# Kernel tuning notes

Hardware: AMD Instinct MI355X
Metric: run time of the kernel (lower is better)

## Reference

```python
import jax, jax.numpy as jnp
import numpy as np

EPS = 1e-08
N_READS = 4
CELL_WIDTH = 64


def setup_inputs() -> dict:
    key = jax.random.key(0)
    ks = jax.random.split(key, 6)
    B, N, W, R = 8, 2048, CELL_WIDTH, N_READS
    memory = jax.random.normal(ks[0], (B, N, W), dtype=jnp.float32)
    controls = jax.random.normal(ks[1], (B, R * W + R + R * 3), dtype=jnp.float32)
    ww = jax.random.uniform(ks[2], (B, N), dtype=jnp.float32)
    write_weights = ww / ww.sum(-1, keepdims=True)  # simplex, as a DNC write head yields
    prev_links = jax.random.uniform(ks[3], (B, N, N), dtype=jnp.float32)
    prev_precedence = jax.random.uniform(ks[4], (B, N), dtype=jnp.float32)
    rw = jax.random.uniform(ks[5], (B, R, N), dtype=jnp.float32)
    prev_read_weights = rw / rw.sum(-1, keepdims=True)
    return {
        "memory": memory,
        "controls": controls,
        "write_weights": write_weights,
        "prev_links": prev_links,
        "prev_precedence": prev_precedence,
        "prev_read_weights": prev_read_weights,
    }


def reference(memory, controls, write_weights, prev_links, prev_precedence, prev_read_weights):
    B, N, W = memory.shape
    R = N_READS
    # --- split controls per self.shapes: [[R, W], R, [R, 3]] ---
    keys = controls[:, : R * W].reshape(B, R, W)
    betas = 1.0 + jax.nn.softplus(controls[:, R * W : R * W + R])  # [B, R]
    gates = jax.nn.softmax(controls[:, R * W + R :].reshape(B, R, 3), axis=-1)
    # --- content addressing: cosine similarity + softmax ---
    key_norm = jnp.linalg.norm(keys, axis=-1)    # [B, R]
    mem_norm = jnp.linalg.norm(memory, axis=-1)  # [B, N]
    dots = jnp.einsum("bnw,brw->brn", memory, keys)
    scores = dots / (key_norm[:, :, None] * mem_norm[:, None, :] + EPS)
    content_weights = jax.nn.softmax(scores * betas[:, :, None], axis=-1)  # [B, R, N]
    # --- temporal link matrix update ---
    wt_i = write_weights[:, :, None]          # [B, N, 1]
    wt_j = write_weights[:, None, :]          # [B, 1, N]
    pt_j = prev_precedence[:, None, :]        # [B, 1, N]
    diag_mask = 1.0 - jnp.eye(N, dtype=memory.dtype)
    links = ((1.0 - wt_i - wt_j) * prev_links + wt_i * pt_j) * diag_mask  # [B, N, N]
    # --- forward / backward weightings from prev read weights ---
    forward_weights = jnp.einsum("bij,brj->bri", links, prev_read_weights)
    backward_weights = jnp.einsum("bij,bri->brj", links, prev_read_weights)
    # --- mix via read modes ---
    read_weights = (
        gates[..., 0:1] * forward_weights
        + gates[..., 1:2] * backward_weights
        + gates[..., 2:3] * content_weights
    )  # [B, R, N]
    # --- read vector ---
    read_vector = jnp.einsum("bnw,brn->brw", memory, read_weights)  # [B, R, W]
    return read_vector
```

## Files before the change

### kernel.cpp

```cpp
#include <hip/hip_runtime.h>
#include <math.h>

#define BB 8
#define NN 2048
#define WWID 64
#define RNUM 4
#define CTRL 272
#define EPSF 1e-8f
#define TI 32
#define TILES 64
#define CQ 4

__device__ __forceinline__ float wred_sum(float v){
#pragma unroll
  for (int m=1;m<64;m<<=1) v += __shfl_xor(v,m);
  return v;
}

__global__ __launch_bounds__(256) void k1_prep(
    const float* __restrict__ mem, const float* __restrict__ ctr,
    const float* __restrict__ ww, const float* __restrict__ prw,
    const float* __restrict__ L,
    float* __restrict__ scores, float* __restrict__ a_arr,
    float* __restrict__ Ldiag){
  int wid = threadIdx.x >> 6, lane = threadIdx.x & 63;
  int g = blockIdx.x * 4 + wid;
  int b = g >> 11, n = g & (NN-1);
  float m = mem[((size_t)(b*NN + n))*WWID + lane];
  const float* cb = ctr + b*CTRL;
  float k0 = cb[0*WWID+lane], k1 = cb[1*WWID+lane];
  float k2 = cb[2*WWID+lane], k3 = cb[3*WWID+lane];
  float s0 = m*m;
  float d0 = m*k0, d1 = m*k1, d2 = m*k2, d3 = m*k3;
  float q0 = k0*k0, q1 = k1*k1, q2 = k2*k2, q3 = k3*k3;
#pragma unroll
  for (int t=1;t<64;t<<=1){
    s0 += __shfl_xor(s0,t);
    d0 += __shfl_xor(d0,t); d1 += __shfl_xor(d1,t);
    d2 += __shfl_xor(d2,t); d3 += __shfl_xor(d3,t);
    q0 += __shfl_xor(q0,t); q1 += __shfl_xor(q1,t);
    q2 += __shfl_xor(q2,t); q3 += __shfl_xor(q3,t);
  }
  if (lane==0){
    float mn = sqrtf(s0);
    float be[4];
#pragma unroll
    for (int r=0;r<4;r++){
      float x = cb[RNUM*WWID + r];
      be[r] = 1.f + (x > 20.f ? x : log1pf(expf(x)));
    }
    scores[(b*RNUM+0)*NN+n] = d0*be[0]/(sqrtf(q0)*mn + EPSF);
    scores[(b*RNUM+1)*NN+n] = d1*be[1]/(sqrtf(q1)*mn + EPSF);
    scores[(b*RNUM+2)*NN+n] = d2*be[2]/(sqrtf(q2)*mn + EPSF);
    scores[(b*RNUM+3)*NN+n] = d3*be[3]/(sqrtf(q3)*mn + EPSF);
    Ldiag[b*NN+n] = L[((size_t)(b*NN+n))*NN + n];
  }
  if (lane < RNUM){
    int r = lane;
    a_arr[(b*RNUM+r)*NN+n] = (1.f - ww[b*NN+n]) * prw[(b*RNUM+r)*NN+n];
  }
}

__global__ __launch_bounds__(1024) void k2_head(
    const float* __restrict__ ctr, const float* __restrict__ scores,
    const float* __restrict__ ww, const float* __restrict__ prec,
    const float* __restrict__ prw, float* __restrict__ scal){
  __shared__ float redS[16], redT[16], redE[16];
  int tid=threadIdx.x, wid=tid>>6, lane=tid&63;
  int b = blockIdx.x>>2, r = blockIdx.x&3;
  const float* sc = scores + (size_t)(b*RNUM+r)*NN;
  const float* pr = prw    + (size_t)(b*RNUM+r)*NN;
  float s0=sc[tid], s1=sc[tid+1024];
  float p0=pr[tid], p1=pr[tid+1024];
  float lE = expf(s0)+expf(s1);
  float lS = prec[b*NN+tid]*p0 + prec[b*NN+tid+1024]*p1;
  float lT = ww[b*NN+tid]*p0   + ww[b*NN+tid+1024]*p1;
  lE=wred_sum(lE); lS=wred_sum(lS); lT=wred_sum(lT);
  if (lane==0){ redE[wid]=lE; redS[wid]=lS; redT[wid]=lT; }
  __syncthreads();
  if (tid==0){
    float S=0.f,T=0.f,E=0.f;
#pragma unroll
    for(int i=0;i<16;i++){ S+=redS[i]; T+=redT[i]; E+=redE[i]; }
    const float* cb = ctr + b*CTRL;
    float c0 = cb[RNUM*WWID + RNUM + r*3 + 0];
    float c1 = cb[RNUM*WWID + RNUM + r*3 + 1];
    float c2 = cb[RNUM*WWID + RNUM + r*3 + 2];
    float mg = fmaxf(c0, fmaxf(c1, c2));
    float e0 = expf(c0-mg), e1 = expf(c1-mg), e2 = expf(c2-mg);
    float inv3 = 1.f/(e0+e1+e2);
    float* s = &scal[(b*RNUM+r)*8];
    s[0]=e0*inv3; s[1]=e1*inv3; s[2]=e2*inv3;
    s[3]=S; s[4]=T; s[5]=1.f/E;
  }
}

__global__ __launch_bounds__(256) void k3_links(
    const float* __restrict__ L, const float* __restrict__ ww,
    const float* __restrict__ prw, const float* __restrict__ a_arr,
    float* __restrict__ fwd_part, float* __restrict__ part){
  __shared__ float lrow[TI][16];
  __shared__ float lcol[4096];
  int tid = threadIdx.x, wid = tid>>6, lane = tid&63;
  int bid = blockIdx.x;
  int b   = bid >> 8;
  int rem = bid & 255;
  int tile = rem >> 2, cq = rem & 3;
  int i0 = tile*TI, jbase = cq*512;
  if (tid < TI){
    int i = i0 + tid;
    lrow[tid][0] = ww[b*NN + i];
#pragma unroll
    for (int r=0;r<RNUM;r++){
      lrow[tid][4+r] = a_arr[(b*RNUM+r)*NN + i];
      lrow[tid][8+r] = prw[(b*RNUM+r)*NN + i];
    }
  }
  __syncthreads();
  float accf[32];
#pragma unroll
  for (int k=0;k<32;k++) accf[k]=0.f;

  for (int c=0;c<2;c++){
    int j0 = jbase + c*256 + lane*4;
    float4 a4[4], p4[4];
#pragma unroll
    for (int r=0;r<4;r++){
      a4[r] = *reinterpret_cast<const float4*>(&a_arr[(b*RNUM+r)*NN + j0]);
      p4[r] = *reinterpret_cast<const float4*>(&prw[(b*RNUM+r)*NN + j0]);
    }
    float4 wwj = *reinterpret_cast<const float4*>(&ww[b*NN + j0]);
    float4 cacc[4];
#pragma unroll
    for (int r=0;r<4;r++){ cacc[r].x=0.f; cacc[r].y=0.f; cacc[r].z=0.f; cacc[r].w=0.f; }

#pragma unroll
    for (int rr=0; rr<8; rr++){
      int lr = wid*8 + rr;
      int i  = i0 + lr;
      float wwi = lrow[lr][0];
      float4 ai4 = *reinterpret_cast<const float4*>(&lrow[lr][4]);
      float4 pi4 = *reinterpret_cast<const float4*>(&lrow[lr][8]);
      float4 L4 = *reinterpret_cast<const float4*>(&L[((size_t)(b*NN + i))*NN + j0]);
#pragma unroll
      for (int r=0;r<4;r++){
        float4 ar = a4[r], pr = p4[r];
        float mx_ = fmaf(-wwi, pr.x, ar.x);
        float my_ = fmaf(-wwi, pr.y, ar.y);
        float mz_ = fmaf(-wwi, pr.z, ar.z);
        float mw_ = fmaf(-wwi, pr.w, ar.w);
        float s = accf[rr*4+r];
        s = fmaf(L4.x, mx_, s); s = fmaf(L4.y, my_, s);
        s = fmaf(L4.z, mz_, s); s = fmaf(L4.w, mw_, s);
        accf[rr*4+r] = s;
        float ai = (r==0)?ai4.x:((r==1)?ai4.y:((r==2)?ai4.z:ai4.w));
        float pi = (r==0)?pi4.x:((r==1)?pi4.y:((r==2)?pi4.z:pi4.w));
        float nx_ = fmaf(-wwj.x, pi, ai);
        float ny_ = fmaf(-wwj.y, pi, ai);
        float nz_ = fmaf(-wwj.z, pi, ai);
        float nw_ = fmaf(-wwj.w, pi, ai);
        cacc[r].x = fmaf(L4.x, nx_, cacc[r].x);
        cacc[r].y = fmaf(L4.y, ny_, cacc[r].y);
        cacc[r].z = fmaf(L4.z, nz_, cacc[r].z);
        cacc[r].w = fmaf(L4.w, nw_, cacc[r].w);
      }
    }
    __syncthreads();
#pragma unroll
    for (int r=0;r<4;r++)
      *reinterpret_cast<float4*>(&lcol[wid*1024 + r*256 + lane*4]) = cacc[r];
    __syncthreads();
    float4 v; v.x=0.f; v.y=0.f; v.z=0.f; v.w=0.f;
#pragma unroll
    for (int w=0;w<4;w++){
      float4 t = *reinterpret_cast<const float4*>(&lcol[w*1024 + wid*256 + lane*4]);
      v.x+=t.x; v.y+=t.y; v.z+=t.z; v.w+=t.w;
    }
    *reinterpret_cast<float4*>(
      &part[((size_t)((b*TILES+tile)*RNUM + wid))*NN + jbase + c*256 + lane*4]) = v;
  }

#pragma unroll
  for (int k=0;k<32;k++) accf[k] += __shfl_xor(accf[k], 32);
#pragma unroll
  for (int h=16; h>=1; h>>=1){
#pragma unroll
    for (int i=0;i<h;i++){
      float a = accf[i], bb = accf[i+h];
      bool up = (lane & h) != 0;
      float lo = up ? bb : a;
      float hi = up ? a : bb;
      accf[i] = lo + __shfl_xor(hi, h);
    }
  }
  if (lane < 32){
    int k = lane;
    fwd_part[((size_t)(b*CQ + cq)*RNUM + (k&3))*NN + i0 + wid*8 + (k>>2)] = accf[0];
  }
}

__global__ __launch_bounds__(256) void k45_combine_read(
    const float* __restrict__ part, const float* __restrict__ fwd_part,
    const float* __restrict__ scores, const float* __restrict__ scal,
    const float* __restrict__ ww, const float* __restrict__ prec,
    const float* __restrict__ prw, const float* __restrict__ Ldiag,
    const float* __restrict__ mem, float* __restrict__ out){
  __shared__ float rwl[256];
  int tid = threadIdx.x;
  int b = blockIdx.x >> 5, rem = blockIdx.x & 31;
  int r = rem >> 3, nb = rem & 7;
  int n = nb*256 + tid;
  const float* s = &scal[(b*RNUM+r)*8];
  float g0=s[0], g1=s[1], g2=s[2], S=s[3], T=s[4], inv=s[5];
  const float* pp = part + ((size_t)(b*TILES)*RNUM + r)*NN + n;
  float b0=0.f,b1=0.f,b2=0.f,b3=0.f;
  for (int t=0;t<TILES;t+=4){
    b0 += pp[(size_t)(t+0)*RNUM*NN];
    b1 += pp[(size_t)(t+1)*RNUM*NN];
    b2 += pp[(size_t)(t+2)*RNUM*NN];
    b3 += pp[(size_t)(t+3)*RNUM*NN];
  }
  float bsum = (b0+b1)+(b2+b3);
  float fsum = 0.f;
#pragma unroll
  for (int cq=0;cq<CQ;cq++)
    fsum += fwd_part[((size_t)(b*CQ + cq)*RNUM + r)*NN + n];
  float wwn = ww[b*NN+n], pn = prec[b*NN+n], prn = prw[(b*RNUM+r)*NN+n];
  float Lnn = Ldiag[b*NN+n];
  float diag = (fmaf(-2.f*wwn, Lnn, Lnn) + wwn*pn) * prn;
  float fwd = fsum + wwn*S - diag;
  float bwd = bsum + pn*T - diag;
  float content = expf(scores[(b*RNUM+r)*NN+n]) * inv;
  rwl[tid] = g0*fwd + g1*bwd + g2*content;
  __syncthreads();
  int w = tid>>6, lane = tid&63;
  float acc = 0.f;
  const float* mp = mem + ((size_t)(b*NN + nb*256 + w*64))*WWID + lane;
#pragma unroll 4
  for (int q=0; q<64; q++)
    acc = fmaf(mp[(size_t)q*WWID], rwl[w*64+q], acc);
  atomicAdd(&out[(b*RNUM+r)*WWID + lane], acc);
}

extern "C" void kernel_launch(void* const* d_in, const int* in_sizes, int n_in,
                              void* d_out, int out_size, void* d_ws, size_t ws_size,
                              hipStream_t stream){
  const float* mem  = (const float*)d_in[0];
  const float* ctr  = (const float*)d_in[1];
  const float* ww   = (const float*)d_in[2];
  const float* L    = (const float*)d_in[3];
  const float* prec = (const float*)d_in[4];
  const float* prw  = (const float*)d_in[5];
  float* out = (float*)d_out;
  float* w = (float*)d_ws;

  float* scores   = w;
  float* a_arr    = scores + BB*RNUM*NN;
  float* Ldiag    = a_arr + BB*RNUM*NN;
  float* scal     = Ldiag + BB*NN;
  float* fwd_part = scal + 256;
  float* part     = fwd_part + BB*CQ*RNUM*NN;

  hipMemsetAsync(out, 0, (size_t)BB*RNUM*WWID*sizeof(float), stream);
  k1_prep<<<BB*NN/4, 256, 0, stream>>>(mem, ctr, ww, prw, L, scores, a_arr, Ldiag);
  k2_head<<<BB*RNUM, 1024, 0, stream>>>(ctr, scores, ww, prec, prw, scal);
  k3_links<<<BB*TILES*CQ, 256, 0, stream>>>(L, ww, prw, a_arr, fwd_part, part);
  k45_combine_read<<<BB*RNUM*8, 256, 0, stream>>>(part, fwd_part, scores, scal,
                                                  ww, prec, prw, Ldiag, mem, out);
}
```

Measured before the change: 250.0 us.

## Fuse head reductions into links kernel, zero output in prep, store partials as bf16

The separate head-reduction kernel is folded into the links kernel as 32 extra blocks, and the output memset moves into the first block of the prep kernel, which removes two launches. The per-tile backward partials (64 tiles × 4 reads × 2048 × 8 batches) are now written and read as bf16 rather than fp32, halving that intermediate traffic. The risk is lost precision when 64 bf16 partial sums are accumulated. The links kernel's main work reads the full 134 MB link matrix, so the launch and partial-traffic savings are small next to it.

```diff
diff --git a/kernel.cpp b/kernel.cpp
--- a/kernel.cpp
+++ b/kernel.cpp
@@ -1,4 +1,5 @@
 #include <hip/hip_runtime.h>
+#include <hip/hip_bf16.h>
 #include <math.h>
 
 #define BB 8
@@ -10,11 +11,19 @@
 #define TI 32
 #define TILES 64
 #define CQ 4
+#define K3BLKS (BB*TILES*CQ)
 
 __device__ __forceinline__ float wred_sum(float v){
 #pragma unroll
   for (int m=1;m<64;m<<=1) v += __shfl_xor(v,m);
   return v;
+}
+__device__ __forceinline__ unsigned short f2bf(float f){
+  __hip_bfloat16 h = __float2bfloat16(f);
+  return *reinterpret_cast<unsigned short*>(&h);
+}
+__device__ __forceinline__ float bf2f(unsigned short u){
+  return __uint_as_float(((unsigned)u) << 16);
 }
 
 __global__ __launch_bounds__(256) void k1_prep(
@@ -22,8 +31,14 @@
     const float* __restrict__ ww, const float* __restrict__ prw,
     const float* __restrict__ L,
     float* __restrict__ scores, float* __restrict__ a_arr,
-    float* __restrict__ Ldiag){
-  int wid = threadIdx.x >> 6, lane = threadIdx.x & 63;
+    float* __restrict__ Ldiag, float* __restrict__ out){
+  int tid = threadIdx.x;
+  if (blockIdx.x == 0){
+    float4 z = {0.f,0.f,0.f,0.f};
+    reinterpret_cast<float4*>(out)[tid]       = z;
+    reinterpret_cast<float4*>(out)[tid + 256] = z;
+  }
+  int wid = tid >> 6, lane = tid & 63;
   int g = blockIdx.x * 4 + wid;
   int b = g >> 11, n = g & (NN-1);
   float m = mem[((size_t)(b*NN + n))*WWID + lane];
@@ -61,48 +76,54 @@
   }
 }
 
-__global__ __launch_bounds__(1024) void k2_head(
-    const float* __restrict__ ctr, const float* __restrict__ scores,
-    const float* __restrict__ ww, const float* __restrict__ prec,
-    const float* __restrict__ prw, float* __restrict__ scal){
-  __shared__ float redS[16], redT[16], redE[16];
-  int tid=threadIdx.x, wid=tid>>6, lane=tid&63;
-  int b = blockIdx.x>>2, r = blockIdx.x&3;
-  const float* sc = scores + (size_t)(b*RNUM+r)*NN;
-  const float* pr = prw    + (size_t)(b*RNUM+r)*NN;
-  float s0=sc[tid], s1=sc[tid+1024];
-  float p0=pr[tid], p1=pr[tid+1024];
-  float lE = expf(s0)+expf(s1);
-  float lS = prec[b*NN+tid]*p0 + prec[b*NN+tid+1024]*p1;
-  float lT = ww[b*NN+tid]*p0   + ww[b*NN+tid+1024]*p1;
-  lE=wred_sum(lE); lS=wred_sum(lS); lT=wred_sum(lT);
-  if (lane==0){ redE[wid]=lE; redS[wid]=lS; redT[wid]=lT; }
-  __syncthreads();
-  if (tid==0){
-    float S=0.f,T=0.f,E=0.f;
-#pragma unroll
-    for(int i=0;i<16;i++){ S+=redS[i]; T+=redT[i]; E+=redE[i]; }
-    const float* cb = ctr + b*CTRL;
-    float c0 = cb[RNUM*WWID + RNUM + r*3 + 0];
-    float c1 = cb[RNUM*WWID + RNUM + r*3 + 1];
-    float c2 = cb[RNUM*WWID + RNUM + r*3 + 2];
-    float mg = fmaxf(c0, fmaxf(c1, c2));
-    float e0 = expf(c0-mg), e1 = expf(c1-mg), e2 = expf(c2-mg);
-    float inv3 = 1.f/(e0+e1+e2);
-    float* s = &scal[(b*RNUM+r)*8];
-    s[0]=e0*inv3; s[1]=e1*inv3; s[2]=e2*inv3;
-    s[3]=S; s[4]=T; s[5]=1.f/E;
-  }
-}
-
-__global__ __launch_bounds__(256) void k3_links(
+__global__ __launch_bounds__(256) void k23_links_head(
     const float* __restrict__ L, const float* __restrict__ ww,
     const float* __restrict__ prw, const float* __restrict__ a_arr,
-    float* __restrict__ fwd_part, float* __restrict__ part){
+    const float* __restrict__ ctr, const float* __restrict__ scores,
+    const float* __restrict__ prec,
+    float* __restrict__ fwd_part, unsigned short* __restrict__ part,
+    float* __restrict__ scal){
   __shared__ float lrow[TI][16];
   __shared__ float lcol[4096];
+  __shared__ float red[3][4];
   int tid = threadIdx.x, wid = tid>>6, lane = tid&63;
   int bid = blockIdx.x;
+
+  if (bid >= K3BLKS){
+    int idx = bid - K3BLKS;
+    int b = idx >> 2, r = idx & 3;
+    const float* sc = scores + (size_t)(b*RNUM+r)*NN;
+    const float* pr = prw    + (size_t)(b*RNUM+r)*NN;
+    float lE=0.f, lS=0.f, lT=0.f;
+#pragma unroll
+    for (int k=0;k<8;k++){
+      int n = tid + k*256;
+      float p = pr[n];
+      lE += expf(sc[n]);
+      lS = fmaf(prec[b*NN+n], p, lS);
+      lT = fmaf(ww[b*NN+n],   p, lT);
+    }
+    lE=wred_sum(lE); lS=wred_sum(lS); lT=wred_sum(lT);
+    if (lane==0){ red[0][wid]=lE; red[1][wid]=lS; red[2][wid]=lT; }
+    __syncthreads();
+    if (tid==0){
+      float E = red[0][0]+red[0][1]+red[0][2]+red[0][3];
+      float S = red[1][0]+red[1][1]+red[1][2]+red[1][3];
+      float T = red[2][0]+red[2][1]+red[2][2]+red[2][3];
+      const float* cb = ctr + b*CTRL;
+      float c0 = cb[RNUM*WWID + RNUM + r*3 + 0];
+      float c1 = cb[RNUM*WWID + RNUM + r*3 + 1];
+      float c2 = cb[RNUM*WWID + RNUM + r*3 + 2];
+      float mg = fmaxf(c0, fmaxf(c1, c2));
+      float e0 = expf(c0-mg), e1 = expf(c1-mg), e2 = expf(c2-mg);
+      float inv3 = 1.f/(e0+e1+e2);
+      float* s = &scal[(b*RNUM+r)*8];
+      s[0]=e0*inv3; s[1]=e1*inv3; s[2]=e2*inv3;
+      s[3]=S; s[4]=T; s[5]=1.f/E;
+    }
+    return;
+  }
+
   int b   = bid >> 8;
   int rem = bid & 255;
   int tile = rem >> 2, cq = rem & 3;
@@ -176,8 +197,10 @@
       float4 t = *reinterpret_cast<const float4*>(&lcol[w*1024 + wid*256 + lane*4]);
       v.x+=t.x; v.y+=t.y; v.z+=t.z; v.w+=t.w;
     }
-    *reinterpret_cast<float4*>(
-      &part[((size_t)((b*TILES+tile)*RNUM + wid))*NN + jbase + c*256 + lane*4]) = v;
+    ushort4 sv;
+    sv.x = f2bf(v.x); sv.y = f2bf(v.y); sv.z = f2bf(v.z); sv.w = f2bf(v.w);
+    *reinterpret_cast<ushort4*>(
+      &part[((size_t)((b*TILES+tile)*RNUM + wid))*NN + jbase + c*256 + lane*4]) = sv;
   }
 
 #pragma unroll
@@ -200,7 +223,7 @@
 }
 
 __global__ __launch_bounds__(256) void k45_combine_read(
-    const float* __restrict__ part, const float* __restrict__ fwd_part,
+    const unsigned short* __restrict__ part, const float* __restrict__ fwd_part,
     const float* __restrict__ scores, const float* __restrict__ scal,
     const float* __restrict__ ww, const float* __restrict__ prec,
     const float* __restrict__ prw, const float* __restrict__ Ldiag,
@@ -212,13 +235,13 @@
   int n = nb*256 + tid;
   const float* s = &scal[(b*RNUM+r)*8];
   float g0=s[0], g1=s[1], g2=s[2], S=s[3], T=s[4], inv=s[5];
-  const float* pp = part + ((size_t)(b*TILES)*RNUM + r)*NN + n;
+  const unsigned short* pp = part + ((size_t)(b*TILES)*RNUM + r)*NN + n;
   float b0=0.f,b1=0.f,b2=0.f,b3=0.f;
   for (int t=0;t<TILES;t+=4){
-    b0 += pp[(size_t)(t+0)*RNUM*NN];
-    b1 += pp[(size_t)(t+1)*RNUM*NN];
-    b2 += pp[(size_t)(t+2)*RNUM*NN];
-    b3 += pp[(size_t)(t+3)*RNUM*NN];
+    b0 += bf2f(pp[(size_t)(t+0)*RNUM*NN]);
+    b1 += bf2f(pp[(size_t)(t+1)*RNUM*NN]);
+    b2 += bf2f(pp[(size_t)(t+2)*RNUM*NN]);
+    b3 += bf2f(pp[(size_t)(t+3)*RNUM*NN]);
   }
   float bsum = (b0+b1)+(b2+b3);
   float fsum = 0.f;
@@ -259,12 +282,11 @@
   float* Ldiag    = a_arr + BB*RNUM*NN;
   float* scal     = Ldiag + BB*NN;
   float* fwd_part = scal + 256;
-  float* part     = fwd_part + BB*CQ*RNUM*NN;
-
-  hipMemsetAsync(out, 0, (size_t)BB*RNUM*WWID*sizeof(float), stream);
-  k1_prep<<<BB*NN/4, 256, 0, stream>>>(mem, ctr, ww, prw, L, scores, a_arr, Ldiag);
-  k2_head<<<BB*RNUM, 1024, 0, stream>>>(ctr, scores, ww, prec, prw, scal);
-  k3_links<<<BB*TILES*CQ, 256, 0, stream>>>(L, ww, prw, a_arr, fwd_part, part);
+  unsigned short* part = (unsigned short*)(fwd_part + BB*CQ*RNUM*NN);
+
+  k1_prep<<<BB*NN/4, 256, 0, stream>>>(mem, ctr, ww, prw, L, scores, a_arr, Ldiag, out);
+  k23_links_head<<<K3BLKS + BB*RNUM, 256, 0, stream>>>(L, ww, prw, a_arr, ctr, scores,
+                                                       prec, fwd_part, part, scal);
   k45_combine_read<<<BB*RNUM*8, 256, 0, stream>>>(part, fwd_part, scores, scal,
                                                   ww, prec, prw, Ldiag, mem, out);
 }
```

Result: faster. 244.5 us (-2.2%).
